# Performance work log

Measured on AMD Instinct MI355X. Metric: run time of the kernel, lower is better.

Reference implementation:

```python
import jax, jax.numpy as jnp
import numpy as np

SIGMA_P = 0.01  # sigma_p from __init__
T = 2_000_000   # number of time samples / PMD steps


def _pauli():
    # Pauli spin matrices used by Czegledi (2016) rotation model
    return jnp.array([[[1, 0], [0, -1]],
                      [[0, 1], [1, 0]],
                      [[0, -1j], [1j, 0]]], dtype=jnp.complex64)


def setup_inputs() -> dict:
    key = jax.random.key(0)
    k1, k2, k3, k4 = jax.random.split(key, 4)
    signal_re = jax.random.normal(k1, (T, 2), dtype=jnp.float32)
    signal_im = jax.random.normal(k2, (T, 2), dtype=jnp.float32)
    alphas = jax.random.normal(k3, (T, 3), dtype=jnp.float32)  # raw N(0,1); scaled by SIGMA_P inside reference
    # initial Jones matrix J_k1 built from a random unit 4-vector (as in __init__)
    g = jax.random.normal(k4, (4,), dtype=jnp.float32)
    a0 = g / jnp.linalg.norm(g)
    theta0 = jnp.arccos(a0[0])
    alpha = a0[1:] / jnp.sin(theta0) * theta0
    theta = jnp.linalg.norm(alpha)
    a = (alpha / theta).astype(jnp.complex64)
    J0 = (jnp.eye(2, dtype=jnp.complex64) * jnp.cos(theta)
          - 1j * jnp.einsum('a,aij->ij', a, _pauli()) * jnp.sin(theta))
    return {"signal_re": signal_re, "signal_im": signal_im, "alphas": alphas,
            "J0_re": jnp.real(J0), "J0_im": jnp.imag(J0)}


def reference(signal_re, signal_im, alphas, J0_re, J0_im):
    pauli = _pauli()
    al = alphas * SIGMA_P                      # [T,3] per-step rotation vectors
    thetas = jnp.linalg.norm(al, axis=1)       # [T]
    a = (al / thetas[:, None]).astype(jnp.complex64)   # [T,3] unit axes
    eye = jnp.eye(2, dtype=jnp.complex64)
    # per-step incremental Jones matrices: J_delta[k] = I*cos(th) - i*(a.sigma)*sin(th)
    J_delta = (eye[None, :, :] * jnp.cos(thetas)[:, None, None]
               - 1j * jnp.einsum('ka,aij->kij', a, pauli) * jnp.sin(thetas)[:, None, None])  # [T,2,2]
    # cumulative left-product: chain[k] = J_delta[k] @ ... @ J_delta[0]
    chain = jax.lax.associative_scan(lambda x, y: jnp.matmul(y, x), J_delta)  # [T,2,2]
    J0 = (J0_re + 1j * J0_im).astype(jnp.complex64)
    J_k = jnp.einsum('kij,jl->kil', chain, J0)  # [T,2,2] time-varying Jones matrices
    signal = (signal_re + 1j * signal_im).astype(jnp.complex64)  # [T,2]
    return jnp.einsum('kij,kj->ki', J_k, signal)  # [T,2] complex64
```

## Files before the change

kernel.cpp:

```cpp
#include <hip/hip_runtime.h>
#include <hip/hip_bf16.h>

#define BLK 256
#define CH 8

__device__ __forceinline__ float4 qmul(const float4 A, const float4 B) {
    return make_float4(
        A.x*B.x - A.y*B.y - A.z*B.z - A.w*B.w,
        A.x*B.y + B.x*A.y + A.z*B.w - A.w*B.z,
        A.x*B.z + B.x*A.z + A.w*B.y - A.y*B.w,
        A.x*B.w + B.x*A.w + A.y*B.z - A.z*B.y);
}

__device__ __forceinline__ float4 qid() { return make_float4(1.f, 0.f, 0.f, 0.f); }

__device__ __forceinline__ float4 qnorm(const float4 q) {
    float n = rsqrtf(q.x*q.x + q.y*q.y + q.z*q.z + q.w*q.w);
    return make_float4(q.x*n, q.y*n, q.z*n, q.w*n);
}

__device__ __forceinline__ float4 dquat(float a0, float a1, float a2) {
    float x = a0 * 0.01f, y = a1 * 0.01f, z = a2 * 0.01f;
    float t2 = x*x + y*y + z*z;
    float c = 1.f - t2 * (0.5f - t2 * (1.f / 24.f));
    float f = 1.f - t2 * ((1.f / 6.f) - t2 * (1.f / 120.f));
    return make_float4(c, f*x, f*y, f*z);
}

__device__ __forceinline__ float4 qapply(const float4 m, float s0r, float s1r,
                                         float s0i, float s1i) {
    float w = m.x, v1 = m.y, v2 = m.z, v3 = m.w;
    return make_float4(
        w*s0r + v1*s0i - v3*s1r + v2*s1i,
        w*s0i - v1*s0r - v2*s1r - v3*s1i,
        v3*s0r + v2*s0i + w*s1r - v1*s1i,
        v3*s0i - v2*s0r + w*s1i + v1*s1r);
}

__device__ __forceinline__ float4 shfl_up4(const float4 v, int s) {
    return make_float4(__shfl_up(v.x, s), __shfl_up(v.y, s),
                       __shfl_up(v.z, s), __shfl_up(v.w, s));
}
__device__ __forceinline__ float4 shfl_down4(const float4 v, int s) {
    return make_float4(__shfl_down(v.x, s), __shfl_down(v.y, s),
                       __shfl_down(v.z, s), __shfl_down(v.w, s));
}

__device__ __forceinline__ float4 wave_prod_desc(float4 c) {
    #pragma unroll
    for (int s = 1; s < 64; s <<= 1) {
        float4 u = shfl_down4(c, s);
        c = qmul(u, c);
    }
    return c;
}

__device__ __forceinline__ float4 wave_scan_incl(float4 v, int lane) {
    #pragma unroll
    for (int s = 1; s < 64; s <<= 1) {
        float4 u = shfl_up4(v, s);
        if (lane >= s) v = qmul(v, u);
    }
    return v;
}

__device__ __forceinline__ float4 chunk_prod(const float* __restrict__ al,
                                             long long t, long long T,
                                             long long nchunk) {
    if (t >= nchunk) return qid();
    float4 q = qid();
    if ((t + 1) * CH <= T) {
        const float4* ap = reinterpret_cast<const float4*>(al) + (size_t)t * 6;
        float4 v0 = ap[0], v1 = ap[1], v2 = ap[2];
        float4 v3 = ap[3], v4 = ap[4], v5 = ap[5];
        q = dquat(v0.x, v0.y, v0.z);
        q = qmul(dquat(v0.w, v1.x, v1.y), q);
        q = qmul(dquat(v1.z, v1.w, v2.x), q);
        q = qmul(dquat(v2.y, v2.z, v2.w), q);
        q = qmul(dquat(v3.x, v3.y, v3.z), q);
        q = qmul(dquat(v3.w, v4.x, v4.y), q);
        q = qmul(dquat(v4.z, v4.w, v5.x), q);
        q = qmul(dquat(v5.y, v5.z, v5.w), q);
    } else {
        for (int j = 0; j < CH; ++j) {
            long long k = t * CH + j;
            if (k < T) q = qmul(dquat(al[k*3], al[k*3+1], al[k*3+2]), q);
        }
    }
    return qnorm(q);
}

__device__ __forceinline__ float4 chunk_quats(const float* __restrict__ al,
                                              long long t, long long T,
                                              long long nchunk, float4* d, bool& full) {
    float4 q = qid();
    full = false;
    if (t >= nchunk) {
        #pragma unroll
        for (int j = 0; j < CH; ++j) d[j] = qid();
        return q;
    }
    if ((t + 1) * CH <= T) {
        full = true;
        const float4* ap = reinterpret_cast<const float4*>(al) + (size_t)t * 6;
        float4 v0 = ap[0], v1 = ap[1], v2 = ap[2];
        float4 v3 = ap[3], v4 = ap[4], v5 = ap[5];
        d[0] = dquat(v0.x, v0.y, v0.z);
        d[1] = dquat(v0.w, v1.x, v1.y);
        d[2] = dquat(v1.z, v1.w, v2.x);
        d[3] = dquat(v2.y, v2.z, v2.w);
        d[4] = dquat(v3.x, v3.y, v3.z);
        d[5] = dquat(v3.w, v4.x, v4.y);
        d[6] = dquat(v4.z, v4.w, v5.x);
        d[7] = dquat(v5.y, v5.z, v5.w);
    } else {
        #pragma unroll
        for (int j = 0; j < CH; ++j) {
            long long k = t * CH + j;
            d[j] = (k < T) ? dquat(al[k*3], al[k*3+1], al[k*3+2]) : qid();
        }
    }
    #pragma unroll
    for (int j = 0; j < CH; ++j) q = qmul(d[j], q);
    return qnorm(q);
}

__device__ __forceinline__ void apply_and_store(
    const float4* d, float4 run, bool full, long long t, long long T,
    const float* __restrict__ sre, const float* __restrict__ sim,
    float* __restrict__ outf) {
    if (full) {
        const float4* rp = reinterpret_cast<const float4*>(sre) + (size_t)t * 4;
        const float4* ip = reinterpret_cast<const float4*>(sim) + (size_t)t * 4;
        float4* op = reinterpret_cast<float4*>(outf) + (size_t)t * 4;
        float4 r0 = rp[0], r1 = rp[1], r2 = rp[2], r3 = rp[3];
        float4 i0 = ip[0], i1 = ip[1], i2 = ip[2], i3 = ip[3];
        float4 p0, p1;
        run = qmul(d[0], run); p0 = qapply(run, r0.x, r0.y, i0.x, i0.y);
        run = qmul(d[1], run); p1 = qapply(run, r0.z, r0.w, i0.z, i0.w);
        op[0] = make_float4(p0.x, p0.z, p1.x, p1.z);
        run = qmul(d[2], run); p0 = qapply(run, r1.x, r1.y, i1.x, i1.y);
        run = qmul(d[3], run); p1 = qapply(run, r1.z, r1.w, i1.z, i1.w);
        op[1] = make_float4(p0.x, p0.z, p1.x, p1.z);
        run = qmul(d[4], run); p0 = qapply(run, r2.x, r2.y, i2.x, i2.y);
        run = qmul(d[5], run); p1 = qapply(run, r2.z, r2.w, i2.z, i2.w);
        op[2] = make_float4(p0.x, p0.z, p1.x, p1.z);
        run = qmul(d[6], run); p0 = qapply(run, r3.x, r3.y, i3.x, i3.y);
        run = qmul(d[7], run); p1 = qapply(run, r3.z, r3.w, i3.z, i3.w);
        op[3] = make_float4(p0.x, p0.z, p1.x, p1.z);
    } else {
        float2* op2 = reinterpret_cast<float2*>(outf);
        #pragma unroll
        for (int j = 0; j < CH; ++j) {
            long long k = t * CH + j;
            if (k < T) {
                run = qmul(d[j], run);
                float4 p = qapply(run, sre[k*2], sre[k*2+1], sim[k*2], sim[k*2+1]);
                op2[k] = make_float2(p.x, p.z);
            }
        }
    }
}

__global__ void __launch_bounds__(BLK) pmd_k1(
    const float* __restrict__ al, float4* __restrict__ A,
    long long T, long long nchunk) {
    __shared__ float4 sW[BLK / 64];
    const int tid = threadIdx.x, lane = tid & 63, wid = tid >> 6;
    const long long t = (long long)blockIdx.x * BLK + tid;
    float4 q = chunk_prod(al, t, T, nchunk);
    float4 wp = wave_prod_desc(q);
    if (lane == 0) sW[wid] = wp;
    __syncthreads();
    if (tid == 0) {
        float4 a = qmul(sW[1], sW[0]);
        a = qmul(sW[2], a);
        a = qmul(sW[3], a);
        A[blockIdx.x] = qnorm(a);
    }
}

__global__ void __launch_bounds__(BLK) pmd_k2(
    const float* __restrict__ al, const float* __restrict__ sre,
    const float* __restrict__ sim, const float* __restrict__ j0re,
    const float* __restrict__ j0im, const float4* __restrict__ A,
    float* __restrict__ outf, long long T, long long nchunk) {
    __shared__ float4 sW[BLK / 64];
    __shared__ float4 sexcl;
    const int tid = threadIdx.x, lane = tid & 63, wid = tid >> 6;
    const int b = blockIdx.x;
    const long long t = (long long)b * BLK + tid;

    float4 d[CH];
    bool full;
    float4 q = chunk_quats(al, t, T, nchunk, d, full);

    float4 v = wave_scan_incl(q, lane);
    if (lane == 63) sW[wid] = v;

    if (tid < 64) {
        float4 sp = qid();
        if (b > 0) {
            int top = b - 1;
            int base = (top >> 6) << 6;
            for (;;) {
                int j = base + lane;
                float4 contrib = (j <= top) ? A[j] : qid();
                float4 wp = wave_prod_desc(contrib);
                sp = qmul(sp, wp);
                if (base == 0) break;
                top = base - 1;
                base -= 64;
            }
        }
        if (lane == 0) {
            float4 q0 = make_float4(j0re[0], -j0im[0], -j0im[1], -j0re[1]);
            sexcl = qnorm(qmul(sp, q0));
        }
    }
    __syncthreads();

    float4 P = qid();
    for (int w = 0; w < wid; ++w) P = qmul(sW[w], P);
    float4 vprev = shfl_up4(v, 1);
    float4 Xv = (lane == 0) ? P : qmul(vprev, P);
    float4 run = qmul(Xv, sexcl);
    if (t < nchunk)
        apply_and_store(d, run, full, t, T, sre, sim, outf);
}

__global__ void __launch_bounds__(BLK) pmd_mono(
    const float* __restrict__ al, const float* __restrict__ sre,
    const float* __restrict__ sim, const float* __restrict__ j0re,
    const float* __restrict__ j0im, float* __restrict__ outf, long long T) {
    __shared__ float4 sW[BLK / 64];
    __shared__ float4 sbase;
    const int tid = threadIdx.x, lane = tid & 63, wid = tid >> 6;
    if (tid == 0)
        sbase = make_float4(j0re[0], -j0im[0], -j0im[1], -j0re[1]);
    __syncthreads();
    const long long nchunk = (T + CH - 1) / CH;
    for (long long c0 = 0; c0 < nchunk; c0 += BLK) {
        const long long t = c0 + tid;
        float4 d[CH];
        bool full;
        float4 q = chunk_quats(al, t, T, nchunk, d, full);
        float4 v = wave_scan_incl(q, lane);
        if (lane == 63) sW[wid] = v;
        __syncthreads();
        float4 P = qid();
        for (int w = 0; w < wid; ++w) P = qmul(sW[w], P);
        float4 vprev = shfl_up4(v, 1);
        float4 Xv = (lane == 0) ? P : qmul(vprev, P);
        float4 base = sbase;
        __syncthreads();
        if (tid == BLK - 1) sbase = qnorm(qmul(qmul(v, P), base));
        if (t < nchunk) {
            float4 run = qmul(Xv, base);
            apply_and_store(d, run, full, t, T, sre, sim, outf);
        }
        __syncthreads();
    }
}

extern "C" void kernel_launch(void* const* d_in, const int* in_sizes, int n_in,
                              void* d_out, int out_size, void* d_ws, size_t ws_size,
                              hipStream_t stream) {
    const float* sre  = (const float*)d_in[0];
    const float* sim  = (const float*)d_in[1];
    const float* al   = (const float*)d_in[2];
    const float* j0re = (const float*)d_in[3];
    const float* j0im = (const float*)d_in[4];
    float* outf = (float*)d_out;
    long long T = (long long)in_sizes[2] / 3;
    if (T <= 0) return;

    long long nchunk = (T + CH - 1) / CH;
    long long nblkLL = (nchunk + BLK - 1) / BLK;
    size_t need = (size_t)nblkLL * sizeof(float4);

    if (ws_size >= need && nblkLL <= 0x7fffffff) {
        int nblk = (int)nblkLL;
        float4* A = (float4*)d_ws;
        pmd_k1<<<nblk, BLK, 0, stream>>>(al, A, T, nchunk);
        pmd_k2<<<nblk, BLK, 0, stream>>>(al, sre, sim, j0re, j0im, A, outf, T, nchunk);
    } else {
        pmd_mono<<<1, BLK, 0, stream>>>(al, sre, sim, j0re, j0im, outf, T);
    }
}
```

Baseline: 34.71 us.

## Fuse two-pass scan into single cooperative kernel with grid-wide sync

Replaces the separate block-reduction and apply kernels with one cooperative kernel. It computes chunk quaternions once, publishes block aggregates, waits on a grid sync, then applies the prefix and stores the outputs. This removes one kernel launch and the second read of the rotation inputs, since the per-chunk quaternions stay in registers across the sync. It relies on all blocks being co-resident, which the launch-bounds hint targets, and falls back to the two-kernel path if the cooperative launch fails. Grid sync overhead and register pressure from holding the chunk data are the costs.

```diff
diff --git a/kernel.cpp b/kernel.cpp
--- a/kernel.cpp
+++ b/kernel.cpp
@@ -1,5 +1,8 @@
 #include <hip/hip_runtime.h>
 #include <hip/hip_bf16.h>
+#include <hip/hip_cooperative_groups.h>
+
+namespace cg = cooperative_groups;
 
 #define BLK 256
 #define CH 8
@@ -62,32 +65,6 @@
         if (lane >= s) v = qmul(v, u);
     }
     return v;
-}
-
-__device__ __forceinline__ float4 chunk_prod(const float* __restrict__ al,
-                                             long long t, long long T,
-                                             long long nchunk) {
-    if (t >= nchunk) return qid();
-    float4 q = qid();
-    if ((t + 1) * CH <= T) {
-        const float4* ap = reinterpret_cast<const float4*>(al) + (size_t)t * 6;
-        float4 v0 = ap[0], v1 = ap[1], v2 = ap[2];
-        float4 v3 = ap[3], v4 = ap[4], v5 = ap[5];
-        q = dquat(v0.x, v0.y, v0.z);
-        q = qmul(dquat(v0.w, v1.x, v1.y), q);
-        q = qmul(dquat(v1.z, v1.w, v2.x), q);
-        q = qmul(dquat(v2.y, v2.z, v2.w), q);
-        q = qmul(dquat(v3.x, v3.y, v3.z), q);
-        q = qmul(dquat(v3.w, v4.x, v4.y), q);
-        q = qmul(dquat(v4.z, v4.w, v5.x), q);
-        q = qmul(dquat(v5.y, v5.z, v5.w), q);
-    } else {
-        for (int j = 0; j < CH; ++j) {
-            long long k = t * CH + j;
-            if (k < T) q = qmul(dquat(al[k*3], al[k*3+1], al[k*3+2]), q);
-        }
-    }
-    return qnorm(q);
 }
 
 __device__ __forceinline__ float4 chunk_quats(const float* __restrict__ al,
@@ -123,6 +100,14 @@
     #pragma unroll
     for (int j = 0; j < CH; ++j) q = qmul(d[j], q);
     return qnorm(q);
+}
+
+__device__ __forceinline__ float4 chunk_prod(const float* __restrict__ al,
+                                             long long t, long long T,
+                                             long long nchunk) {
+    float4 d[CH];
+    bool full;
+    return chunk_quats(al, t, T, nchunk, d, full);
 }
 
 __device__ __forceinline__ void apply_and_store(
@@ -162,6 +147,68 @@
     }
 }
 
+__device__ __forceinline__ float4 spine_prefix(const float4* __restrict__ A,
+                                               int b, int lane) {
+    float4 sp = qid();
+    if (b > 0) {
+        int top = b - 1;
+        int base = (top >> 6) << 6;
+        for (;;) {
+            int j = base + lane;
+            float4 contrib = (j <= top) ? A[j] : qid();
+            float4 wp = wave_prod_desc(contrib);
+            sp = qmul(sp, wp);
+            if (base == 0) break;
+            top = base - 1;
+            base -= 64;
+        }
+    }
+    return sp;
+}
+
+__global__ void __launch_bounds__(BLK, 4) pmd_coop(
+    const float* __restrict__ al, const float* __restrict__ sre,
+    const float* __restrict__ sim, const float* __restrict__ j0re,
+    const float* __restrict__ j0im, float* __restrict__ outf,
+    float4* __restrict__ A, long long T, long long nchunk) {
+    __shared__ float4 sW[BLK / 64];
+    __shared__ float4 sexcl;
+    const int tid = threadIdx.x, lane = tid & 63, wid = tid >> 6;
+    const int b = blockIdx.x;
+    const long long t = (long long)b * BLK + tid;
+
+    float4 d[CH];
+    bool full;
+    float4 q = chunk_quats(al, t, T, nchunk, d, full);
+    float4 v = wave_scan_incl(q, lane);
+    if (lane == 63) sW[wid] = v;
+    __syncthreads();
+    if (tid == 0) {
+        float4 a = qmul(sW[1], sW[0]);
+        a = qmul(sW[2], a);
+        a = qmul(sW[3], a);
+        A[b] = qnorm(a);
+    }
+    float4 P = qid();
+    for (int w = 0; w < wid; ++w) P = qmul(sW[w], P);
+    float4 vprev = shfl_up4(v, 1);
+    float4 Xv = (lane == 0) ? P : qmul(vprev, P);
+
+    cg::this_grid().sync();
+
+    if (tid < 64) {
+        float4 sp = spine_prefix(A, b, lane);
+        if (lane == 0) {
+            float4 q0 = make_float4(j0re[0], -j0im[0], -j0im[1], -j0re[1]);
+            sexcl = qnorm(qmul(sp, q0));
+        }
+    }
+    __syncthreads();
+    float4 run = qmul(Xv, sexcl);
+    if (t < nchunk)
+        apply_and_store(d, run, full, t, T, sre, sim, outf);
+}
+
 __global__ void __launch_bounds__(BLK) pmd_k1(
     const float* __restrict__ al, float4* __restrict__ A,
     long long T, long long nchunk) {
@@ -194,25 +241,11 @@
     float4 d[CH];
     bool full;
     float4 q = chunk_quats(al, t, T, nchunk, d, full);
-
     float4 v = wave_scan_incl(q, lane);
     if (lane == 63) sW[wid] = v;
 
     if (tid < 64) {
-        float4 sp = qid();
-        if (b > 0) {
-            int top = b - 1;
-            int base = (top >> 6) << 6;
-            for (;;) {
-                int j = base + lane;
-                float4 contrib = (j <= top) ? A[j] : qid();
-                float4 wp = wave_prod_desc(contrib);
-                sp = qmul(sp, wp);
-                if (base == 0) break;
-                top = base - 1;
-                base -= 64;
-            }
-        }
+        float4 sp = spine_prefix(A, b, lane);
         if (lane == 0) {
             float4 q0 = make_float4(j0re[0], -j0im[0], -j0im[1], -j0re[1]);
             sexcl = qnorm(qmul(sp, q0));
@@ -282,8 +315,21 @@
     if (ws_size >= need && nblkLL <= 0x7fffffff) {
         int nblk = (int)nblkLL;
         float4* A = (float4*)d_ws;
-        pmd_k1<<<nblk, BLK, 0, stream>>>(al, A, T, nchunk);
-        pmd_k2<<<nblk, BLK, 0, stream>>>(al, sre, sim, j0re, j0im, A, outf, T, nchunk);
+        bool done = false;
+        if (nblk <= 1024) {
+            void* args[] = { (void*)&al, (void*)&sre, (void*)&sim, (void*)&j0re,
+                             (void*)&j0im, (void*)&outf, (void*)&A,
+                             (void*)&T, (void*)&nchunk };
+            hipError_t e = hipLaunchCooperativeKernel(
+                reinterpret_cast<const void*>(&pmd_coop),
+                dim3(nblk), dim3(BLK), args, 0, stream);
+            done = (e == hipSuccess);
+        }
+        if (!done) {
+            pmd_k1<<<nblk, BLK, 0, stream>>>(al, A, T, nchunk);
+            pmd_k2<<<nblk, BLK, 0, stream>>>(al, sre, sim, j0re, j0im, A,
+                                             outf, T, nchunk);
+        }
     } else {
         pmd_mono<<<1, BLK, 0, stream>>>(al, sre, sim, j0re, j0im, outf, T);
     }
```

Result: slower. 104.9 us (+202.2%).

## Replace per-block serial prefix lookback with a dedicated block-prefix scan kernel

Applied to the files above, without the earlier changes.

Previously each block in the second pass walked back over every earlier block aggregate in 64-wide chunks, which costs work quadratic in the block count. A small single-block kernel now scans the block aggregates once, folds in J0, and writes one exclusive prefix per block. The apply kernel then reads its prefix directly. This adds a third launch and a serial single-block step, and the two-kernel path is now limited to at most 4096 blocks.

```diff
diff --git a/kernel.cpp b/kernel.cpp
--- a/kernel.cpp
+++ b/kernel.cpp
@@ -62,32 +62,6 @@
         if (lane >= s) v = qmul(v, u);
     }
     return v;
-}
-
-__device__ __forceinline__ float4 chunk_prod(const float* __restrict__ al,
-                                             long long t, long long T,
-                                             long long nchunk) {
-    if (t >= nchunk) return qid();
-    float4 q = qid();
-    if ((t + 1) * CH <= T) {
-        const float4* ap = reinterpret_cast<const float4*>(al) + (size_t)t * 6;
-        float4 v0 = ap[0], v1 = ap[1], v2 = ap[2];
-        float4 v3 = ap[3], v4 = ap[4], v5 = ap[5];
-        q = dquat(v0.x, v0.y, v0.z);
-        q = qmul(dquat(v0.w, v1.x, v1.y), q);
-        q = qmul(dquat(v1.z, v1.w, v2.x), q);
-        q = qmul(dquat(v2.y, v2.z, v2.w), q);
-        q = qmul(dquat(v3.x, v3.y, v3.z), q);
-        q = qmul(dquat(v3.w, v4.x, v4.y), q);
-        q = qmul(dquat(v4.z, v4.w, v5.x), q);
-        q = qmul(dquat(v5.y, v5.z, v5.w), q);
-    } else {
-        for (int j = 0; j < CH; ++j) {
-            long long k = t * CH + j;
-            if (k < T) q = qmul(dquat(al[k*3], al[k*3+1], al[k*3+2]), q);
-        }
-    }
-    return qnorm(q);
 }
 
 __device__ __forceinline__ float4 chunk_quats(const float* __restrict__ al,
@@ -123,6 +97,14 @@
     #pragma unroll
     for (int j = 0; j < CH; ++j) q = qmul(d[j], q);
     return qnorm(q);
+}
+
+__device__ __forceinline__ float4 chunk_prod(const float* __restrict__ al,
+                                             long long t, long long T,
+                                             long long nchunk) {
+    float4 d[CH];
+    bool full;
+    return chunk_quats(al, t, T, nchunk, d, full);
 }
 
 __device__ __forceinline__ void apply_and_store(
@@ -180,13 +162,40 @@
     }
 }
 
+template<int EPT>
 __global__ void __launch_bounds__(BLK) pmd_k2(
+    const float4* __restrict__ A, float4* __restrict__ EB,
+    const float* __restrict__ j0re, const float* __restrict__ j0im, int nblk) {
+    __shared__ float4 sW[BLK / 64];
+    const int tid = threadIdx.x, lane = tid & 63, wid = tid >> 6;
+    const int t0 = tid * EPT;
+    float4 excl[EPT];
+    float4 run = qid();
+    #pragma unroll
+    for (int e = 0; e < EPT; ++e) {
+        excl[e] = run;
+        if (t0 + e < nblk) run = qmul(A[t0 + e], run);
+    }
+    float4 v = wave_scan_incl(run, lane);
+    if (lane == 63) sW[wid] = v;
+    __syncthreads();
+    float4 P = qid();
+    for (int w = 0; w < wid; ++w) P = qmul(sW[w], P);
+    float4 vprev = shfl_up4(v, 1);
+    float4 texcl = (lane == 0) ? P : qmul(vprev, P);
+    float4 q0 = make_float4(j0re[0], -j0im[0], -j0im[1], -j0re[1]);
+    float4 base = qmul(texcl, q0);
+    #pragma unroll
+    for (int e = 0; e < EPT; ++e) {
+        if (t0 + e < nblk) EB[t0 + e] = qnorm(qmul(excl[e], base));
+    }
+}
+
+__global__ void __launch_bounds__(BLK) pmd_k3(
     const float* __restrict__ al, const float* __restrict__ sre,
-    const float* __restrict__ sim, const float* __restrict__ j0re,
-    const float* __restrict__ j0im, const float4* __restrict__ A,
+    const float* __restrict__ sim, const float4* __restrict__ EB,
     float* __restrict__ outf, long long T, long long nchunk) {
     __shared__ float4 sW[BLK / 64];
-    __shared__ float4 sexcl;
     const int tid = threadIdx.x, lane = tid & 63, wid = tid >> 6;
     const int b = blockIdx.x;
     const long long t = (long long)b * BLK + tid;
@@ -194,37 +203,14 @@
     float4 d[CH];
     bool full;
     float4 q = chunk_quats(al, t, T, nchunk, d, full);
-
     float4 v = wave_scan_incl(q, lane);
     if (lane == 63) sW[wid] = v;
-
-    if (tid < 64) {
-        float4 sp = qid();
-        if (b > 0) {
-            int top = b - 1;
-            int base = (top >> 6) << 6;
-            for (;;) {
-                int j = base + lane;
-                float4 contrib = (j <= top) ? A[j] : qid();
-                float4 wp = wave_prod_desc(contrib);
-                sp = qmul(sp, wp);
-                if (base == 0) break;
-                top = base - 1;
-                base -= 64;
-            }
-        }
-        if (lane == 0) {
-            float4 q0 = make_float4(j0re[0], -j0im[0], -j0im[1], -j0re[1]);
-            sexcl = qnorm(qmul(sp, q0));
-        }
-    }
-    __syncthreads();
-
+    __syncthreads();
     float4 P = qid();
     for (int w = 0; w < wid; ++w) P = qmul(sW[w], P);
     float4 vprev = shfl_up4(v, 1);
     float4 Xv = (lane == 0) ? P : qmul(vprev, P);
-    float4 run = qmul(Xv, sexcl);
+    float4 run = qmul(Xv, EB[b]);
     if (t < nchunk)
         apply_and_store(d, run, full, t, T, sre, sim, outf);
 }
@@ -277,13 +263,19 @@
 
     long long nchunk = (T + CH - 1) / CH;
     long long nblkLL = (nchunk + BLK - 1) / BLK;
-    size_t need = (size_t)nblkLL * sizeof(float4);
-
-    if (ws_size >= need && nblkLL <= 0x7fffffff) {
+    size_t need = (size_t)(2 * nblkLL) * sizeof(float4);
+
+    if (ws_size >= need && nblkLL <= (long long)BLK * 16) {
         int nblk = (int)nblkLL;
-        float4* A = (float4*)d_ws;
+        float4* A  = (float4*)d_ws;
+        float4* EB = A + nblk;
         pmd_k1<<<nblk, BLK, 0, stream>>>(al, A, T, nchunk);
-        pmd_k2<<<nblk, BLK, 0, stream>>>(al, sre, sim, j0re, j0im, A, outf, T, nchunk);
+        if      (nblk <= BLK)      pmd_k2<1> <<<1, BLK, 0, stream>>>(A, EB, j0re, j0im, nblk);
+        else if (nblk <= 2 * BLK)  pmd_k2<2> <<<1, BLK, 0, stream>>>(A, EB, j0re, j0im, nblk);
+        else if (nblk <= 4 * BLK)  pmd_k2<4> <<<1, BLK, 0, stream>>>(A, EB, j0re, j0im, nblk);
+        else if (nblk <= 8 * BLK)  pmd_k2<8> <<<1, BLK, 0, stream>>>(A, EB, j0re, j0im, nblk);
+        else                       pmd_k2<16><<<1, BLK, 0, stream>>>(A, EB, j0re, j0im, nblk);
+        pmd_k3<<<nblk, BLK, 0, stream>>>(al, sre, sim, EB, outf, T, nchunk);
     } else {
         pmd_mono<<<1, BLK, 0, stream>>>(al, sre, sim, j0re, j0im, outf, T);
     }
```

Result: faster. 28.88 us (median of 2 runs) (-16.8%).
